# Kernel optimization log

Hardware: AMD Instinct MI355X
Metric: run time of the kernel (lower is better)

## Reference

```python
import jax, jax.numpy as jnp
import numpy as np

EPS = 1e-6

def _rmsnorm(x, w):
    # RMSNorm in float32 as in the torch module, then rescale by weight
    xf = x.astype(jnp.float32)
    y = xf * jax.lax.rsqrt(jnp.mean(xf * xf, axis=-1, keepdims=True) + EPS)
    return y.astype(x.dtype) * w

def setup_inputs() -> dict:
    key = jax.random.key(0)
    k0, k1, k2 = jax.random.split(key, 3)
    B, T, C = 2, 1024, 256
    x = jax.random.normal(k0, (B, T, C), jnp.float32)
    w_qkv = jax.random.normal(k1, (3 * C, C), jnp.float32) / np.float32(np.sqrt(C))
    w_proj = jax.random.normal(k2, (C, C), jnp.float32) / np.float32(np.sqrt(C))
    qn_w = jnp.ones((2,), jnp.float32)
    kn_w = jnp.ones((2,), jnp.float32)
    return {"x": x, "w_qkv": w_qkv, "w_proj": w_proj, "qn_w": qn_w, "kn_w": kn_w}

def reference(x, w_qkv, w_proj, qn_w, kn_w):
    B, T, C = x.shape
    HD = 2                      # head_dim forced to 2 by GPTConfig invariant
    H = C // HD                 # n_head = n_embd // 2
    qkv = x @ w_qkv.T           # (B, T, 3C); Linear has bias=False
    q, k, v = jnp.split(qkv, 3, axis=-1)
    heads = lambda t: t.reshape(B, T, H, HD).transpose(0, 2, 1, 3)  # (B,H,T,2)
    q = _rmsnorm(heads(q), qn_w)
    k = _rmsnorm(heads(k), kn_w)
    v = heads(v)
    scale = np.float32(1.0 / np.sqrt(HD))
    att = jnp.einsum('bhtd,bhsd->bhts', q, k) * scale   # (B,H,T,T)
    causal = jnp.tril(jnp.ones((T, T), bool))
    att = jnp.where(causal, att, jnp.float32(-1e30))
    att = jax.nn.softmax(att, axis=-1)
    y = jnp.einsum('bhts,bhsd->bhtd', att, v)           # (B,H,T,2)
    y = y.transpose(0, 2, 1, 3).reshape(B, T, C)
    return y @ w_proj.T
```

## Files before the change

### kernel.cpp

```cpp
#include <hip/hip_runtime.h>
#include <hip/hip_bf16.h>

#define T_SEQ   1024
#define C_DIM   256
#define H_HEADS 128
#define NTOK    2048
#define BH      256

typedef unsigned short u16;
typedef unsigned int   u32;
typedef __attribute__((ext_vector_type(8))) short bf16x8;
typedef __attribute__((ext_vector_type(4))) float f32x4;

__device__ __forceinline__ float bf2f(u16 u) {
  return __uint_as_float(((u32)u) << 16);
}
__device__ __forceinline__ u16 f2bf(float f) {
  u32 u = __float_as_uint(f);
  u32 r = u + 0x7fffu + ((u >> 16) & 1u);
  return (u16)(r >> 16);
}

#define LDS_K 72

__device__ __forceinline__ void stage_hilo(
    const float* __restrict__ src, int row0, int k0, int tid,
    u16 (*hi)[LDS_K], u16 (*lo)[LDS_K])
{
#pragma unroll
  for (int it = 0; it < 4; ++it) {
    int idx = it * 256 + tid;
    int r = idx >> 4, c4 = (idx & 15) * 4;
    float4 g = *(const float4*)&src[(row0 + r) * C_DIM + k0 + c4];
    ushort4 h4, l4;
    h4.x = f2bf(g.x); l4.x = f2bf(g.x - bf2f(h4.x));
    h4.y = f2bf(g.y); l4.y = f2bf(g.y - bf2f(h4.y));
    h4.z = f2bf(g.z); l4.z = f2bf(g.z - bf2f(h4.z));
    h4.w = f2bf(g.w); l4.w = f2bf(g.w - bf2f(h4.w));
    *(ushort4*)&hi[r][c4] = h4;
    *(ushort4*)&lo[r][c4] = l4;
  }
}

__device__ __forceinline__ void mfma_chunk(
    const u16 (*sXhi)[LDS_K], const u16 (*sXlo)[LDS_K],
    const u16 (*sWhi)[LDS_K], const u16 (*sWlo)[LDS_K],
    int lane, int w, f32x4* acc)
{
  const int fr = lane & 15;
  const int ko = (lane >> 4) * 8;
#pragma unroll
  for (int ks = 0; ks < 2; ++ks) {
    const int kk = ks * 32 + ko;
    bf16x8 bhi = *(const bf16x8*)&sWhi[w * 16 + fr][kk];
    bf16x8 blo = *(const bf16x8*)&sWlo[w * 16 + fr][kk];
#pragma unroll
    for (int rt = 0; rt < 4; ++rt) {
      bf16x8 ahi = *(const bf16x8*)&sXhi[rt * 16 + fr][kk];
      bf16x8 alo = *(const bf16x8*)&sXlo[rt * 16 + fr][kk];
      acc[rt] = __builtin_amdgcn_mfma_f32_16x16x32_bf16(alo, bhi, acc[rt], 0, 0, 0);
      acc[rt] = __builtin_amdgcn_mfma_f32_16x16x32_bf16(ahi, blo, acc[rt], 0, 0, 0);
      acc[rt] = __builtin_amdgcn_mfma_f32_16x16x32_bf16(ahi, bhi, acc[rt], 0, 0, 0);
    }
  }
}

__global__ __launch_bounds__(256) void k_qkv(
    const float* __restrict__ x, const float* __restrict__ wqkv,
    const float* __restrict__ qnw, const float* __restrict__ knw,
    float* __restrict__ q, float* __restrict__ kv)
{
  __shared__ u16 sXhi[64][LDS_K], sXlo[64][LDS_K];
  __shared__ u16 sWhi[64][LDS_K], sWlo[64][LDS_K];

  const int tid  = threadIdx.x;
  const int lane = tid & 63;
  const int w    = tid >> 6;
  const int row0 = blockIdx.x * 64;
  const int col0 = blockIdx.y * 64;

  f32x4 acc[4] = {};

  for (int kc = 0; kc < 4; ++kc) {
    stage_hilo(x,    row0, kc * 64, tid, sXhi, sXlo);
    stage_hilo(wqkv, col0, kc * 64, tid, sWhi, sWlo);
    __syncthreads();
    mfma_chunk(sXhi, sXlo, sWhi, sWlo, lane, w, acc);
    __syncthreads();
  }

  const int sec = col0 >> 8;
  const int cg  = col0 + w * 16 + (lane & 15);
  const int d   = cg & 1;
  const int h   = (cg & 255) >> 1;
  const float wn = (sec == 0) ? qnw[d] : (sec == 1) ? knw[d] : 1.f;

#pragma unroll
  for (int rt = 0; rt < 4; ++rt) {
#pragma unroll
    for (int i = 0; i < 4; ++i) {
      float val = acc[rt][i];
      int n = row0 + rt * 16 + (lane >> 4) * 4 + i;
      int b = n >> 10, t = n & 1023;
      int bh = b * H_HEADS + h;
      if (sec < 2) {
        float pv = __shfl_xor(val, 1);
        float rr = rsqrtf(0.5f * (val * val + pv * pv) + 1e-6f);
        val = val * rr * wn;
      }
      if (sec == 0)      q [(bh * T_SEQ + t) * 2 + d]     = val;
      else if (sec == 1) kv[(bh * T_SEQ + t) * 4 + d]     = val;
      else               kv[(bh * T_SEQ + t) * 4 + 2 + d] = val;
    }
  }
}

__global__ __launch_bounds__(256) void k_attn(
    const float* __restrict__ q, const float* __restrict__ kv,
    float* __restrict__ y)
{
  __shared__ float4 skv[T_SEQ];
  __shared__ float  red[4][256][3];

  const int tid  = threadIdx.x;
  const int head = blockIdx.x;
  const int g    = 3 - blockIdx.y;
  const int qb   = g * 256;
  const int S    = qb + 256;
  const int lane = tid & 63;
  const int w    = tid >> 6;

  const float4* kvh = (const float4*)(kv + head * (T_SEQ * 4));
  for (int i = tid; i < S; i += 256) skv[i] = kvh[i];

  const float LS = 0.70710678118f * 1.44269504089f;
  float qx[4], qy[4];
  int   tq[4];
#pragma unroll
  for (int j = 0; j < 4; ++j) {
    tq[j] = qb + j * 64 + lane;
    float2 qv = *(const float2*)&q[(head * T_SEQ + tq[j]) * 2];
    qx[j] = qv.x * LS;
    qy[j] = qv.y * LS;
  }
  __syncthreads();

  float den[4] = {}, nx[4] = {}, ny[4] = {};

  const int cb = qb >> 2;
  const int b0 = w * cb, b1 = b0 + cb;
#pragma unroll 2
  for (int s = b0; s < b1; ++s) {
    float4 kvv = skv[s];
#pragma unroll
    for (int j = 0; j < 4; ++j) {
      float sc = fmaf(qx[j], kvv.x, qy[j] * kvv.y);
      float e  = __builtin_amdgcn_exp2f(sc);
      den[j] += e;
      nx[j] = fmaf(e, kvv.z, nx[j]);
      ny[j] = fmaf(e, kvv.w, ny[j]);
    }
  }
  const int d0 = qb + w * 64;
#pragma unroll 2
  for (int s = d0; s < d0 + 64; ++s) {
    float4 kvv = skv[s];
#pragma unroll
    for (int j = 0; j < 4; ++j) {
      float sc = fmaf(qx[j], kvv.x, qy[j] * kvv.y);
      float e  = __builtin_amdgcn_exp2f(sc);
      e = (s <= tq[j]) ? e : 0.f;
      den[j] += e;
      nx[j] = fmaf(e, kvv.z, nx[j]);
      ny[j] = fmaf(e, kvv.w, ny[j]);
    }
  }

#pragma unroll
  for (int j = 0; j < 4; ++j) {
    red[w][j * 64 + lane][0] = den[j];
    red[w][j * 64 + lane][1] = nx[j];
    red[w][j * 64 + lane][2] = ny[j];
  }
  __syncthreads();

  float dd = 0.f, ax = 0.f, ay = 0.f;
#pragma unroll
  for (int ww = 0; ww < 4; ++ww) {
    dd += red[ww][tid][0];
    ax += red[ww][tid][1];
    ay += red[ww][tid][2];
  }
  float inv = 1.f / dd;
  int b = head >> 7, h = head & 127;
  int t = qb + tid;
  *(float2*)&y[(b * T_SEQ + t) * C_DIM + h * 2] = make_float2(ax * inv, ay * inv);
}

__global__ __launch_bounds__(256) void k_proj(
    const float* __restrict__ y, const float* __restrict__ wproj,
    float* __restrict__ out)
{
  __shared__ u16 sXhi[64][LDS_K], sXlo[64][LDS_K];
  __shared__ u16 sWhi[64][LDS_K], sWlo[64][LDS_K];

  const int tid  = threadIdx.x;
  const int lane = tid & 63;
  const int w    = tid >> 6;
  const int row0 = blockIdx.x * 64;
  const int col0 = blockIdx.y * 64;

  f32x4 acc[4] = {};

  for (int kc = 0; kc < 4; ++kc) {
    stage_hilo(y,     row0, kc * 64, tid, sXhi, sXlo);
    stage_hilo(wproj, col0, kc * 64, tid, sWhi, sWlo);
    __syncthreads();
    mfma_chunk(sXhi, sXlo, sWhi, sWlo, lane, w, acc);
    __syncthreads();
  }

  const int cg = col0 + w * 16 + (lane & 15);
#pragma unroll
  for (int rt = 0; rt < 4; ++rt) {
#pragma unroll
    for (int i = 0; i < 4; ++i) {
      int n = row0 + rt * 16 + (lane >> 4) * 4 + i;
      out[n * C_DIM + cg] = acc[rt][i];
    }
  }
}

extern "C" void kernel_launch(void* const* d_in, const int* in_sizes, int n_in,
                              void* d_out, int out_size, void* d_ws, size_t ws_size,
                              hipStream_t stream) {
  const float* x     = (const float*)d_in[0];
  const float* wqkv  = (const float*)d_in[1];
  const float* wproj = (const float*)d_in[2];
  const float* qnw   = (const float*)d_in[3];
  const float* knw   = (const float*)d_in[4];

  float* ws = (float*)d_ws;
  float* q  = ws;
  float* kv = q  + BH * T_SEQ * 2;
  float* yb = kv + BH * T_SEQ * 4;

  k_qkv <<<dim3(NTOK / 64, 768 / 64),   256, 0, stream>>>(x, wqkv, qnw, knw, q, kv);
  k_attn<<<dim3(BH, 4),                 256, 0, stream>>>(q, kv, yb);
  k_proj<<<dim3(NTOK / 64, C_DIM / 64), 256, 0, stream>>>(yb, wproj, (float*)d_out);
}
```

Measured before the change: 131.6 us.

## Pre-split operands to bf16 hi/lo swizzled tiles and stream via LDS DMA

Measured after the change: 111.6 us. 15.2% less time.

```diff
diff --git a/kernel.cpp b/kernel.cpp
--- a/kernel.cpp
+++ b/kernel.cpp
@@ -1,5 +1,4 @@
 #include <hip/hip_runtime.h>
-#include <hip/hip_bf16.h>
 
 #define T_SEQ   1024
 #define C_DIM   256
@@ -11,6 +10,10 @@
 typedef unsigned int   u32;
 typedef __attribute__((ext_vector_type(8))) short bf16x8;
 typedef __attribute__((ext_vector_type(4))) float f32x4;
+typedef __attribute__((ext_vector_type(2))) float f32x2;
+
+typedef __attribute__((address_space(1))) u32 gu32;
+typedef __attribute__((address_space(3))) u32 lu32;
 
 __device__ __forceinline__ float bf2f(u16 u) {
   return __uint_as_float(((u32)u) << 16);
@@ -21,82 +24,116 @@
   return (u16)(r >> 16);
 }
 
-#define LDS_K 72
-
-__device__ __forceinline__ void stage_hilo(
-    const float* __restrict__ src, int row0, int k0, int tid,
-    u16 (*hi)[LDS_K], u16 (*lo)[LDS_K])
+
+__device__ __forceinline__ void gl_seg(const u16* g, u16* l, int lane) {
+  __builtin_amdgcn_global_load_lds((gu32*)(g + lane * 8), (lu32*)l, 16, 0, 0);
+}
+
+__device__ __forceinline__ bf16x8 ldsf(const u16* plane, int row, int kk) {
+  int off = (row * 128 + kk * 2) ^ ((row & 7) << 4);
+  return *(const bf16x8*)((const char*)plane + off);
+}
+
+__global__ __launch_bounds__(256) void k_pack(
+    const float* __restrict__ x, const float* __restrict__ wq,
+    const float* __restrict__ wp,
+    u16* __restrict__ xh, u16* __restrict__ xl,
+    u16* __restrict__ wqh, u16* __restrict__ wql,
+    u16* __restrict__ wph, u16* __restrict__ wpl)
 {
+  const int bid = blockIdx.x, tid = threadIdx.x;
+  const float* src; u16 *dh, *dl; int ti;
+  if (bid < 128)      { src = x;  dh = xh;  dl = xl;  ti = bid; }
+  else if (bid < 176) { src = wq; dh = wqh; dl = wql; ti = bid - 128; }
+  else                { src = wp; dh = wph; dl = wpl; ti = bid - 176; }
+  const int tr = ti >> 2, kc = ti & 3;
+  char* bh = (char*)dh + (size_t)ti * 8192;
+  char* bl = (char*)dl + (size_t)ti * 8192;
 #pragma unroll
   for (int it = 0; it < 4; ++it) {
     int idx = it * 256 + tid;
     int r = idx >> 4, c4 = (idx & 15) * 4;
-    float4 g = *(const float4*)&src[(row0 + r) * C_DIM + k0 + c4];
+    float4 g = *(const float4*)&src[(tr * 64 + r) * C_DIM + kc * 64 + c4];
     ushort4 h4, l4;
     h4.x = f2bf(g.x); l4.x = f2bf(g.x - bf2f(h4.x));
     h4.y = f2bf(g.y); l4.y = f2bf(g.y - bf2f(h4.y));
     h4.z = f2bf(g.z); l4.z = f2bf(g.z - bf2f(h4.z));
     h4.w = f2bf(g.w); l4.w = f2bf(g.w - bf2f(h4.w));
-    *(ushort4*)&hi[r][c4] = h4;
-    *(ushort4*)&lo[r][c4] = l4;
-  }
-}
-
-__device__ __forceinline__ void mfma_chunk(
-    const u16 (*sXhi)[LDS_K], const u16 (*sXlo)[LDS_K],
-    const u16 (*sWhi)[LDS_K], const u16 (*sWlo)[LDS_K],
-    int lane, int w, f32x4* acc)
-{
-  const int fr = lane & 15;
-  const int ko = (lane >> 4) * 8;
-#pragma unroll
-  for (int ks = 0; ks < 2; ++ks) {
-    const int kk = ks * 32 + ko;
-    bf16x8 bhi = *(const bf16x8*)&sWhi[w * 16 + fr][kk];
-    bf16x8 blo = *(const bf16x8*)&sWlo[w * 16 + fr][kk];
-#pragma unroll
-    for (int rt = 0; rt < 4; ++rt) {
-      bf16x8 ahi = *(const bf16x8*)&sXhi[rt * 16 + fr][kk];
-      bf16x8 alo = *(const bf16x8*)&sXlo[rt * 16 + fr][kk];
-      acc[rt] = __builtin_amdgcn_mfma_f32_16x16x32_bf16(alo, bhi, acc[rt], 0, 0, 0);
-      acc[rt] = __builtin_amdgcn_mfma_f32_16x16x32_bf16(ahi, blo, acc[rt], 0, 0, 0);
-      acc[rt] = __builtin_amdgcn_mfma_f32_16x16x32_bf16(ahi, bhi, acc[rt], 0, 0, 0);
-    }
+    int off = (r * 128 + c4 * 2) ^ ((r & 7) << 4);
+    *(ushort4*)(bh + off) = h4;
+    *(ushort4*)(bl + off) = l4;
   }
 }
 
 __global__ __launch_bounds__(256) void k_qkv(
-    const float* __restrict__ x, const float* __restrict__ wqkv,
+    const u16* __restrict__ xh, const u16* __restrict__ xl,
+    const u16* __restrict__ wh, const u16* __restrict__ wl,
     const float* __restrict__ qnw, const float* __restrict__ knw,
     float* __restrict__ q, float* __restrict__ kv)
 {
-  __shared__ u16 sXhi[64][LDS_K], sXlo[64][LDS_K];
-  __shared__ u16 sWhi[64][LDS_K], sWlo[64][LDS_K];
+  __shared__ __align__(16) u16 lds[2][12288];
 
   const int tid  = threadIdx.x;
   const int lane = tid & 63;
   const int w    = tid >> 6;
-  const int row0 = blockIdx.x * 64;
-  const int col0 = blockIdx.y * 64;
-
-  f32x4 acc[4] = {};
-
+  const int bx   = blockIdx.x, by = blockIdx.y;
+  const int row0 = bx * 32, col0 = by * 64;
+  const int xtb  = (bx >> 1) * 4;
+  const int xho  = (bx & 1) * 2048;
+  const int wtb  = by * 4;
+  const int fr   = lane & 15;
+  const int ko   = (lane >> 4) * 8;
+
+  f32x4 acc[2] = {};
+
+  auto STAGE = [&](int kc, int b) {
+    const u16* gxh = xh + (xtb + kc) * 4096 + xho;
+    const u16* gxl = xl + (xtb + kc) * 4096 + xho;
+    const u16* gwh = wh + (wtb + kc) * 4096;
+    const u16* gwl = wl + (wtb + kc) * 4096;
+    u16* L = lds[b];
+    gl_seg(gxh + w * 512,        L + w * 512,               lane);
+    gl_seg(gxl + w * 512,        L + 2048 + w * 512,        lane);
+    gl_seg(gwh + w * 512,        L + 4096 + w * 512,        lane);
+    gl_seg(gwh + (w + 4) * 512,  L + 4096 + (w + 4) * 512,  lane);
+    gl_seg(gwl + w * 512,        L + 8192 + w * 512,        lane);
+    gl_seg(gwl + (w + 4) * 512,  L + 8192 + (w + 4) * 512,  lane);
+  };
+
+  STAGE(0, 0);
+  __syncthreads();
   for (int kc = 0; kc < 4; ++kc) {
-    stage_hilo(x,    row0, kc * 64, tid, sXhi, sXlo);
-    stage_hilo(wqkv, col0, kc * 64, tid, sWhi, sWlo);
+    if (kc < 3) STAGE(kc + 1, (kc + 1) & 1);
+    const u16* L   = lds[kc & 1];
+    const u16* bXh = L;
+    const u16* bXl = L + 2048;
+    const u16* bWh = L + 4096;
+    const u16* bWl = L + 8192;
+#pragma unroll
+    for (int ks = 0; ks < 2; ++ks) {
+      const int kk = ks * 32 + ko;
+      bf16x8 bhi = ldsf(bWh, w * 16 + fr, kk);
+      bf16x8 blo = ldsf(bWl, w * 16 + fr, kk);
+#pragma unroll
+      for (int rt = 0; rt < 2; ++rt) {
+        bf16x8 ahi = ldsf(bXh, rt * 16 + fr, kk);
+        bf16x8 alo = ldsf(bXl, rt * 16 + fr, kk);
+        acc[rt] = __builtin_amdgcn_mfma_f32_16x16x32_bf16(alo, bhi, acc[rt], 0, 0, 0);
+        acc[rt] = __builtin_amdgcn_mfma_f32_16x16x32_bf16(ahi, blo, acc[rt], 0, 0, 0);
+        acc[rt] = __builtin_amdgcn_mfma_f32_16x16x32_bf16(ahi, bhi, acc[rt], 0, 0, 0);
+      }
+    }
     __syncthreads();
-    mfma_chunk(sXhi, sXlo, sWhi, sWlo, lane, w, acc);
-    __syncthreads();
   }
 
   const int sec = col0 >> 8;
-  const int cg  = col0 + w * 16 + (lane & 15);
+  const int cg  = col0 + w * 16 + fr;
   const int d   = cg & 1;
   const int h   = (cg & 255) >> 1;
   const float wn = (sec == 0) ? qnw[d] : (sec == 1) ? knw[d] : 1.f;
 
 #pragma unroll
-  for (int rt = 0; rt < 4; ++rt) {
+  for (int rt = 0; rt < 2; ++rt) {
 #pragma unroll
     for (int i = 0; i < 4; ++i) {
       float val = acc[rt][i];
@@ -117,7 +154,7 @@
 
 __global__ __launch_bounds__(256) void k_attn(
     const float* __restrict__ q, const float* __restrict__ kv,
-    float* __restrict__ y)
+    u16* __restrict__ yh, u16* __restrict__ yl)
 {
   __shared__ float4 skv[T_SEQ];
   __shared__ float  red[4][256][3];
@@ -134,54 +171,65 @@
   for (int i = tid; i < S; i += 256) skv[i] = kvh[i];
 
   const float LS = 0.70710678118f * 1.44269504089f;
-  float qx[4], qy[4];
-  int   tq[4];
+  float qxs[4], qys[4];
 #pragma unroll
   for (int j = 0; j < 4; ++j) {
-    tq[j] = qb + j * 64 + lane;
-    float2 qv = *(const float2*)&q[(head * T_SEQ + tq[j]) * 2];
-    qx[j] = qv.x * LS;
-    qy[j] = qv.y * LS;
-  }
+    int t = qb + j * 64 + lane;
+    float2 qv = *(const float2*)&q[(head * T_SEQ + t) * 2];
+    qxs[j] = qv.x * LS;
+    qys[j] = qv.y * LS;
+  }
+  f32x2 qx01 = {qxs[0], qxs[1]}, qx23 = {qxs[2], qxs[3]};
+  f32x2 qy01 = {qys[0], qys[1]}, qy23 = {qys[2], qys[3]};
   __syncthreads();
 
-  float den[4] = {}, nx[4] = {}, ny[4] = {};
+  f32x2 den01 = {0.f, 0.f}, den23 = {0.f, 0.f};
+  f32x2 nx01  = {0.f, 0.f}, nx23  = {0.f, 0.f};
+  f32x2 ny01  = {0.f, 0.f}, ny23  = {0.f, 0.f};
 
   const int cb = qb >> 2;
   const int b0 = w * cb, b1 = b0 + cb;
 #pragma unroll 2
   for (int s = b0; s < b1; ++s) {
     float4 kvv = skv[s];
-#pragma unroll
-    for (int j = 0; j < 4; ++j) {
-      float sc = fmaf(qx[j], kvv.x, qy[j] * kvv.y);
-      float e  = __builtin_amdgcn_exp2f(sc);
-      den[j] += e;
-      nx[j] = fmaf(e, kvv.z, nx[j]);
-      ny[j] = fmaf(e, kvv.w, ny[j]);
-    }
-  }
-  const int d0 = qb + w * 64;
+    f32x2 kx = {kvv.x, kvv.x}, ky = {kvv.y, kvv.y};
+    f32x2 kz = {kvv.z, kvv.z}, kw = {kvv.w, kvv.w};
+    f32x2 s01 = __builtin_elementwise_fma(qx01, kx, qy01 * ky);
+    f32x2 s23 = __builtin_elementwise_fma(qx23, kx, qy23 * ky);
+    f32x2 e01 = { __builtin_amdgcn_exp2f(s01.x), __builtin_amdgcn_exp2f(s01.y) };
+    f32x2 e23 = { __builtin_amdgcn_exp2f(s23.x), __builtin_amdgcn_exp2f(s23.y) };
+    den01 += e01; den23 += e23;
+    nx01 = __builtin_elementwise_fma(e01, kz, nx01);
+    nx23 = __builtin_elementwise_fma(e23, kz, nx23);
+    ny01 = __builtin_elementwise_fma(e01, kw, ny01);
+    ny23 = __builtin_elementwise_fma(e23, kw, ny23);
+  }
+  const int d0  = qb + w * 64;
+  const int tqL = qb + lane;
 #pragma unroll 2
   for (int s = d0; s < d0 + 64; ++s) {
     float4 kvv = skv[s];
-#pragma unroll
-    for (int j = 0; j < 4; ++j) {
-      float sc = fmaf(qx[j], kvv.x, qy[j] * kvv.y);
-      float e  = __builtin_amdgcn_exp2f(sc);
-      e = (s <= tq[j]) ? e : 0.f;
-      den[j] += e;
-      nx[j] = fmaf(e, kvv.z, nx[j]);
-      ny[j] = fmaf(e, kvv.w, ny[j]);
-    }
-  }
-
-#pragma unroll
-  for (int j = 0; j < 4; ++j) {
-    red[w][j * 64 + lane][0] = den[j];
-    red[w][j * 64 + lane][1] = nx[j];
-    red[w][j * 64 + lane][2] = ny[j];
-  }
+    f32x2 kx = {kvv.x, kvv.x}, ky = {kvv.y, kvv.y};
+    f32x2 kz = {kvv.z, kvv.z}, kw = {kvv.w, kvv.w};
+    f32x2 s01 = __builtin_elementwise_fma(qx01, kx, qy01 * ky);
+    f32x2 s23 = __builtin_elementwise_fma(qx23, kx, qy23 * ky);
+    f32x2 e01 = { __builtin_amdgcn_exp2f(s01.x), __builtin_amdgcn_exp2f(s01.y) };
+    f32x2 e23 = { __builtin_amdgcn_exp2f(s23.x), __builtin_amdgcn_exp2f(s23.y) };
+    e01.x = (s <= tqL)       ? e01.x : 0.f;
+    e01.y = (s <= tqL + 64)  ? e01.y : 0.f;
+    e23.x = (s <= tqL + 128) ? e23.x : 0.f;
+    e23.y = (s <= tqL + 192) ? e23.y : 0.f;
+    den01 += e01; den23 += e23;
+    nx01 = __builtin_elementwise_fma(e01, kz, nx01);
+    nx23 = __builtin_elementwise_fma(e23, kz, nx23);
+    ny01 = __builtin_elementwise_fma(e01, kw, ny01);
+    ny23 = __builtin_elementwise_fma(e23, kw, ny23);
+  }
+
+  red[w][lane][0]       = den01.x; red[w][lane][1]       = nx01.x; red[w][lane][2]       = ny01.x;
+  red[w][64 + lane][0]  = den01.y; red[w][64 + lane][1]  = nx01.y; red[w][64 + lane][2]  = ny01.y;
+  red[w][128 + lane][0] = den23.x; red[w][128 + lane][1] = nx23.x; red[w][128 + lane][2] = ny23.x;
+  red[w][192 + lane][0] = den23.y; red[w][192 + lane][1] = nx23.y; red[w][192 + lane][2] = ny23.y;
   __syncthreads();
 
   float dd = 0.f, ax = 0.f, ay = 0.f;
@@ -192,42 +240,75 @@
     ay += red[ww][tid][2];
   }
   float inv = 1.f / dd;
-  int b = head >> 7, h = head & 127;
+  float ox = ax * inv, oy = ay * inv;
+  int b = head >> 7, hh = head & 127;
   int t = qb + tid;
-  *(float2*)&y[(b * T_SEQ + t) * C_DIM + h * 2] = make_float2(ax * inv, ay * inv);
+  int n = b * T_SEQ + t;
+  int c = hh * 2;
+  int tile = (n >> 6) * 4 + (c >> 6);
+  int r = n & 63, cc = c & 63;
+  int off = (r * 128 + cc * 2) ^ ((r & 7) << 4);
+  u16 hx = f2bf(ox); float rx = ox - bf2f(hx);
+  u16 hy = f2bf(oy); float ry = oy - bf2f(hy);
+  *(u32*)((char*)yh + (size_t)tile * 8192 + off) = (u32)hx | ((u32)hy << 16);
+  *(u32*)((char*)yl + (size_t)tile * 8192 + off) = (u32)f2bf(rx) | ((u32)f2bf(ry) << 16);
 }
 
 __global__ __launch_bounds__(256) void k_proj(
-    const float* __restrict__ y, const float* __restrict__ wproj,
+    const u16* __restrict__ yh, const u16* __restrict__ yl,
+    const u16* __restrict__ wh, const u16* __restrict__ wl,
     float* __restrict__ out)
 {
-  __shared__ u16 sXhi[64][LDS_K], sXlo[64][LDS_K];
-  __shared__ u16 sWhi[64][LDS_K], sWlo[64][LDS_K];
+  __shared__ __align__(16) u16 lds[2][8192];
 
   const int tid  = threadIdx.x;
   const int lane = tid & 63;
   const int w    = tid >> 6;
-  const int row0 = blockIdx.x * 64;
-  const int col0 = blockIdx.y * 64;
-
-  f32x4 acc[4] = {};
-
+  const int bx   = blockIdx.x, by = blockIdx.y;
+  const int row0 = bx * 32, col0 = by * 32;
+  const int ytb  = (bx >> 1) * 4;
+  const int yho  = (bx & 1) * 2048;
+  const int wtb  = (by >> 1) * 4;
+  const int who  = (by & 1) * 2048;
+  const int fr   = lane & 15;
+  const int ko   = (lane >> 4) * 8;
+
+  f32x4 acc = {};
+
+  auto STAGE = [&](int kc, int b) {
+    u16* L = lds[b];
+    gl_seg(yh + (ytb + kc) * 4096 + yho + w * 512, L + w * 512,        lane);
+    gl_seg(yl + (ytb + kc) * 4096 + yho + w * 512, L + 2048 + w * 512, lane);
+    gl_seg(wh + (wtb + kc) * 4096 + who + w * 512, L + 4096 + w * 512, lane);
+    gl_seg(wl + (wtb + kc) * 4096 + who + w * 512, L + 6144 + w * 512, lane);
+  };
+
+  STAGE(0, 0);
+  __syncthreads();
+  const int ar = (w >> 1) * 16 + fr;
+  const int br = (w & 1) * 16 + fr;
   for (int kc = 0; kc < 4; ++kc) {
-    stage_hilo(y,     row0, kc * 64, tid, sXhi, sXlo);
-    stage_hilo(wproj, col0, kc * 64, tid, sWhi, sWlo);
+    if (kc < 3) STAGE(kc + 1, (kc + 1) & 1);
+    const u16* L = lds[kc & 1];
+#pragma unroll
+    for (int ks = 0; ks < 2; ++ks) {
+      const int kk = ks * 32 + ko;
+      bf16x8 bhi = ldsf(L + 4096, br, kk);
+      bf16x8 blo = ldsf(L + 6144, br, kk);
+      bf16x8 ahi = ldsf(L,        ar, kk);
+      bf16x8 alo = ldsf(L + 2048, ar, kk);
+      acc = __builtin_amdgcn_mfma_f32_16x16x32_bf16(alo, bhi, acc, 0, 0, 0);
+      acc = __builtin_amdgcn_mfma_f32_16x16x32_bf16(ahi, blo, acc, 0, 0, 0);
+      acc = __builtin_amdgcn_mfma_f32_16x16x32_bf16(ahi, bhi, acc, 0, 0, 0);
+    }
     __syncthreads();
-    mfma_chunk(sXhi, sXlo, sWhi, sWlo, lane, w, acc);
-    __syncthreads();
-  }
-
-  const int cg = col0 + w * 16 + (lane & 15);
-#pragma unroll
-  for (int rt = 0; rt < 4; ++rt) {
-#pragma unroll
-    for (int i = 0; i < 4; ++i) {
-      int n = row0 + rt * 16 + (lane >> 4) * 4 + i;
-      out[n * C_DIM + cg] = acc[rt][i];
-    }
+  }
+
+  const int cg = col0 + (w & 1) * 16 + fr;
+#pragma unroll
+  for (int i = 0; i < 4; ++i) {
+    int n = row0 + (w >> 1) * 16 + (lane >> 4) * 4 + i;
+    out[n * C_DIM + cg] = acc[i];
   }
 }
 
@@ -240,12 +321,20 @@
   const float* qnw   = (const float*)d_in[3];
   const float* knw   = (const float*)d_in[4];
 
-  float* ws = (float*)d_ws;
-  float* q  = ws;
-  float* kv = q  + BH * T_SEQ * 2;
-  float* yb = kv + BH * T_SEQ * 4;
-
-  k_qkv <<<dim3(NTOK / 64, 768 / 64),   256, 0, stream>>>(x, wqkv, qnw, knw, q, kv);
-  k_attn<<<dim3(BH, 4),                 256, 0, stream>>>(q, kv, yb);
-  k_proj<<<dim3(NTOK / 64, C_DIM / 64), 256, 0, stream>>>(yb, wproj, (float*)d_out);
-}
+  char* p = (char*)d_ws;
+  float* q  = (float*)p;  p += (size_t)BH * T_SEQ * 2 * 4;
+  float* kv = (float*)p;  p += (size_t)BH * T_SEQ * 4 * 4;
+  u16* xh  = (u16*)p;     p += (size_t)NTOK  * C_DIM * 2;
+  u16* xl  = (u16*)p;     p += (size_t)NTOK  * C_DIM * 2;
+  u16* wqh = (u16*)p;     p += (size_t)768   * C_DIM * 2;
+  u16* wql = (u16*)p;     p += (size_t)768   * C_DIM * 2;
+  u16* wph = (u16*)p;     p += (size_t)C_DIM * C_DIM * 2;
+  u16* wpl = (u16*)p;     p += (size_t)C_DIM * C_DIM * 2;
+  u16* yh  = (u16*)p;     p += (size_t)NTOK  * C_DIM * 2;
+  u16* yl  = (u16*)p;     p += (size_t)NTOK  * C_DIM * 2;
+
+  k_pack<<<192, 256, 0, stream>>>(x, wqkv, wproj, xh, xl, wqh, wql, wph, wpl);
+  k_qkv <<<dim3(64, 12), 256, 0, stream>>>(xh, xl, wqh, wql, qnw, knw, q, kv);
+  k_attn<<<dim3(BH, 4),  256, 0, stream>>>(q, kv, yh, yl);
+  k_proj<<<dim3(64, 8),  256, 0, stream>>>(yh, yl, wph, wpl, (float*)d_out);
+}
```
